# Optimization experiments

Measured on AMD Instinct MI355X. Metric: run time of the kernel, lower is better.

## Reference

```python
import jax, jax.numpy as jnp
import numpy as np

W_KERNEL = 5      # dilation kernel size (w)
K_BG = 0.1        # background weight (k)
RELAX = 5.0       # sigmoid temperature (relax)
INF = 1e4         # 'no zero in column' sentinel (>> image diagonal)
EPS = 1e-7        # DiceLoss eps


def setup_inputs() -> dict:
    key = jax.random.key(0)
    k1, k2 = jax.random.split(key)
    B, H, W = 32, 256, 256
    preds = jax.random.normal(k1, (B, H, W), dtype=jnp.float32)
    targets = (jax.random.uniform(k2, (B, H, W)) > 0.99).astype(jnp.float32)
    return {"preds": preds, "targets": targets}


def _dilate(t, w):
    # cv2.dilate with w x w ones kernel == sliding-window max, SAME padding
    pad = w // 2
    return jax.lax.reduce_window(t, -jnp.inf, jax.lax.max,
                                 (1, w, w), (1, 1, 1),
                                 [(0, 0), (pad, pad), (pad, pad)])


def _vertical_dist(zero_mask):
    # per-column distance (in rows) to nearest zero pixel; [B,H,W] -> [B,H,W]
    B, H, W = zero_mask.shape
    rows = jnp.moveaxis(zero_mask, 1, 0)  # [H,B,W]

    def step(carry, z):
        d = jnp.where(z, 0.0, jnp.minimum(carry + 1.0, INF))
        return d, d

    init = jnp.full((B, W), INF, dtype=jnp.float32)
    _, fwd = jax.lax.scan(step, init, rows)
    _, bwd = jax.lax.scan(step, init, rows[::-1])
    g = jnp.minimum(fwd, bwd[::-1])  # [H,B,W]
    return jnp.moveaxis(g, 0, 1)


def _edt(fat):
    # exact euclidean distance transform (distance to nearest zero pixel),
    # separable two-pass: vertical 1D distance, then horizontal min-plus.
    B, H, W = fat.shape
    g = _vertical_dist(fat == 0)  # [B,H,W]
    col = jnp.arange(W, dtype=jnp.float32)
    off2 = (col[:, None] - col[None, :]) ** 2  # [W_j, W_k]

    def per_img(gi):  # gi: [H,W]
        # d2[i,j] = min_k g[i,k]^2 + (j-k)^2   -> [H,W,W] intermediate
        d2 = jnp.min(gi[:, None, :] ** 2 + off2[None, :, :], axis=-1)
        return jnp.sqrt(d2)

    return jax.lax.map(per_img, g)  # sequential over batch caps memory


def _distance_maps(targets):
    fat = _dilate(targets, W_KERNEL)          # [B,H,W]
    d = _edt(fat)                              # [B,H,W]
    soft = jax.nn.sigmoid(d / RELAX)
    soft = soft - jnp.min(soft, axis=(1, 2), keepdims=True)
    mx = jnp.max(soft, axis=(1, 2), keepdims=True)
    soft = soft / jnp.where(mx > 0, mx, 1.0)
    dm_soft = soft + (1.0 - fat) * K_BG
    has_fg = jnp.max(targets, axis=(1, 2), keepdims=True) > 0
    return jnp.where(has_fg, dm_soft, 1.0 - targets)


def reference(preds, targets):
    p = jax.nn.sigmoid(preds)
    dm = jax.lax.stop_gradient(_distance_maps(targets))  # computed in numpy in torch => constant
    pw = p * dm
    bs = pw.shape[0]
    y_pred = pw.reshape(bs, 1, -1)
    y_true = targets.reshape(bs, 1, -1)
    # smp DiceLoss('binary', from_logits=False): dims=(0,2), smooth=0, eps=1e-7
    inter = jnp.sum(y_pred * y_true, axis=(0, 2))
    card = jnp.sum(y_pred + y_true, axis=(0, 2))
    dice = (2.0 * inter) / jnp.maximum(card, EPS)
    loss = 1.0 - dice
    mask = (jnp.sum(y_true, axis=(0, 2)) > 0).astype(loss.dtype)
    return jnp.mean(loss * mask)
```

## Files before the change

kernel.cpp:

```cpp
#include <hip/hip_runtime.h>
#include <math.h>

#define BB 32
#define HH 256
#define WW 256
#define HW (HH*WW)
#define K_BG 0.1f
#define RELAX 5.0f
#define EPS_D 1e-7

typedef unsigned long long u64;
typedef unsigned short u16;

__device__ __forceinline__ float sigf(float x) { return 1.0f / (1.0f + expf(-x)); }

__device__ __forceinline__ u64 shflx64(u64 x, int s) {
    return (u64)__shfl_xor((unsigned long long)x, s, 64);
}

__global__ void k_maskdil(const float* __restrict__ tg, u64* __restrict__ dmaskT,
                          u64* __restrict__ nzmask) {
    __shared__ u64 nz[20][4];
    __shared__ u64 hd[20][4];
    int blk = blockIdx.x;
    int b = blk >> 4, band = blk & 15;
    int r0 = band * 16;
    int t = threadIdx.x, w = t >> 6;
    const float* img = tg + b * HW;
    for (int rr = 0; rr < 20; ++rr) {
        int rg = r0 + rr - 2;
        float v = (rg >= 0 && rg < HH) ? img[rg * WW + t] : 0.0f;
        u64 bal = __ballot(v != 0.0f);
        if ((t & 63) == 0) nz[rr][w] = bal;
    }
    __syncthreads();
    if (t < 80) {
        int rr = t >> 2, k = t & 3;
        u64 m = nz[rr][k];
        u64 ml = (k > 0) ? nz[rr][k - 1] : 0ULL;
        u64 mr = (k < 3) ? nz[rr][k + 1] : 0ULL;
        hd[rr][k] = m | (m << 1) | (m << 2) | (m >> 1) | (m >> 2)
                  | (ml >> 62) | (ml >> 63) | (mr << 62) | (mr << 63);
    }
    if (t < 64) {
        int rr = t >> 2, k = t & 3;
        nzmask[b * 1024 + (r0 + rr) * 4 + k] = nz[rr + 2][k];
    }
    __syncthreads();
    if (t < 64) {
        int rr = t >> 2, k = t & 3;
        u64 o = hd[rr][k] | hd[rr + 1][k] | hd[rr + 2][k] | hd[rr + 3][k] | hd[rr + 4][k];
        dmaskT[b * 1024 + k * 256 + (r0 + rr)] = o;
    }
}

__global__ __launch_bounds__(256) void k_mega(const float* __restrict__ preds,
                                              const u64* __restrict__ dmaskT,
                                              const u64* __restrict__ nzmask,
                                              float4* __restrict__ part1,
                                              float4* __restrict__ part2) {
    __shared__ u64 colT[4 * 256];
    __shared__ u16 gS[4][WW];
    __shared__ float red[8][4];
    int blk = blockIdx.x;
    int b = blk >> 6, q = blk & 63;
    int i0 = q * 4;
    int tid = threadIdx.x;
    int lane = tid & 63, wv = tid >> 6;
    int j = tid;

    float p[4];
    u64 nzw[4];
    #pragma unroll
    for (int rr = 0; rr < 4; ++rr) {
        p[rr] = preds[(b * HH + i0 + rr) * WW + j];
        nzw[rr] = nzmask[b * 1024 + (i0 + rr) * 4 + (j >> 6)];
    }

    const u64* base = dmaskT + b * 1024;
    const u64 L32 = 0x00000000FFFFFFFFULL, L16 = 0x0000FFFF0000FFFFULL,
              L8  = 0x00FF00FF00FF00FFULL, L4  = 0x0F0F0F0F0F0F0F0FULL,
              L2  = 0x3333333333333333ULL, L1  = 0x5555555555555555ULL;
    #pragma unroll
    for (int w = 0; w < 4; ++w) {
        u64 x = base[w * 256 + wv * 64 + lane];
        u64 pp;
        pp = shflx64(x, 32); x = (lane & 32) ? ((x & ~L32) | ((pp & ~L32) >> 32)) : ((x & L32) | ((pp & L32) << 32));
        pp = shflx64(x, 16); x = (lane & 16) ? ((x & ~L16) | ((pp & ~L16) >> 16)) : ((x & L16) | ((pp & L16) << 16));
        pp = shflx64(x,  8); x = (lane &  8) ? ((x & ~L8 ) | ((pp & ~L8 ) >>  8)) : ((x & L8 ) | ((pp & L8 ) <<  8));
        pp = shflx64(x,  4); x = (lane &  4) ? ((x & ~L4 ) | ((pp & ~L4 ) >>  4)) : ((x & L4 ) | ((pp & L4 ) <<  4));
        pp = shflx64(x,  2); x = (lane &  2) ? ((x & ~L2 ) | ((pp & ~L2 ) >>  2)) : ((x & L2 ) | ((pp & L2 ) <<  2));
        pp = shflx64(x,  1); x = (lane &  1) ? ((x & ~L1 ) | ((pp & ~L1 ) >>  1)) : ((x & L1 ) | ((pp & L1 ) <<  1));
        colT[wv * 256 + w * 64 + lane] = x;
    }
    __syncthreads();

    u64 yw[4];
    #pragma unroll
    for (int g = 0; g < 4; ++g) yw[g] = ~colT[g * 256 + j];

    int g0v[4], fgv[4];
    #pragma unroll
    for (int rr = 0; rr < 4; ++rr) {
        int i = i0 + rr;
        int iw = i >> 6, ib = i & 63;
        u64 lowm  = (2ULL << ib) - 1ULL;
        u64 highm = ~((1ULL << ib) - 1ULL);
        int pu = -1, pd = -1;
        #pragma unroll
        for (int w = 0; w < 4; ++w) {
            u64 m = (w < iw) ? ~0ULL : ((w == iw) ? lowm : 0ULL);
            u64 z = yw[w] & m;
            int cand = (w << 6) + 63 - __clzll(z);
            pu = z ? cand : pu;
        }
        #pragma unroll
        for (int w = 3; w >= 0; --w) {
            u64 m = (w > iw) ? ~0ULL : ((w == iw) ? highm : 0ULL);
            u64 z = yw[w] & m;
            int cand = (w << 6) + (__ffsll((unsigned long long)z) - 1);
            pd = z ? cand : pd;
        }
        int up = (pu >= 0) ? (i - pu) : 10000;
        int dn = (pd >= 0) ? (pd - i) : 10000;
        int g0 = min(min(up, dn), 10000);
        g0v[rr] = g0;
        fgv[rr] = (int)((~yw[iw] >> ib) & 1ULL);
        gS[rr][j] = (u16)g0;
    }
    __syncthreads();

    float vals[8];
    #pragma unroll
    for (int qq = 0; qq < 6; ++qq) vals[qq] = 0.0f;
    vals[6] = 1e30f; vals[7] = 0.0f;
    #pragma unroll
    for (int rr = 0; rr < 4; ++rr) {
        float gv = (float)g0v[rr];
        float best = gv * gv;
        for (int r = 1; r < WW; ++r) {
            float rf = (float)(r * r);
            if (rf >= best) break;
            int jl = j - r, jr = j + r;
            if (jl >= 0) { float v = (float)gS[rr][jl]; best = fminf(best, v * v + rf); }
            if (jr < WW) { float v = (float)gS[rr][jr]; best = fminf(best, v * v + rf); }
        }
        float dv = sqrtf(best);
        float sp = sigf(p[rr]);
        float sd = sigf(dv / RELAX);
        float tv = (float)((nzw[rr] >> (j & 63)) & 1ULL);
        vals[0] += sp * sd * tv;
        vals[1] += sp * tv;
        vals[2] += sp * sd;
        vals[3] += sp;
        vals[4] += fgv[rr] ? 0.0f : sp;
        vals[5] += tv;
        vals[6] = fminf(vals[6], dv);
        vals[7] = fmaxf(vals[7], dv);
    }
    for (int off = 32; off > 0; off >>= 1) {
        #pragma unroll
        for (int qq = 0; qq < 6; ++qq) vals[qq] += __shfl_down(vals[qq], off, 64);
        vals[6] = fminf(vals[6], __shfl_down(vals[6], off, 64));
        vals[7] = fmaxf(vals[7], __shfl_down(vals[7], off, 64));
    }
    if (lane == 0) {
        #pragma unroll
        for (int qq = 0; qq < 8; ++qq) red[qq][wv] = vals[qq];
    }
    __syncthreads();
    if (tid == 0) {
        float s[8];
        #pragma unroll
        for (int qq = 0; qq < 6; ++qq) s[qq] = red[qq][0] + red[qq][1] + red[qq][2] + red[qq][3];
        s[6] = fminf(fminf(red[6][0], red[6][1]), fminf(red[6][2], red[6][3]));
        s[7] = fmaxf(fmaxf(red[7][0], red[7][1]), fmaxf(red[7][2], red[7][3]));
        part1[blk] = make_float4(s[0], s[1], s[2], s[3]);
        part2[blk] = make_float4(s[4], s[5], s[6], s[7]);
    }
}

__global__ void k_img(const float4* __restrict__ part1, const float4* __restrict__ part2,
                      float4* __restrict__ imgout) {
    int b = blockIdx.x, t = threadIdx.x;
    float4 p1 = part1[b * 64 + t];
    float4 p2 = part2[b * 64 + t];
    float vals[8] = {p1.x, p1.y, p1.z, p1.w, p2.x, p2.y, p2.z, p2.w};
    for (int off = 32; off > 0; off >>= 1) {
        #pragma unroll
        for (int qq = 0; qq < 6; ++qq) vals[qq] += __shfl_down(vals[qq], off, 64);
        vals[6] = fminf(vals[6], __shfl_down(vals[6], off, 64));
        vals[7] = fmaxf(vals[7], __shfl_down(vals[7], off, 64));
    }
    if (t == 0) {
        float A = vals[0], Bs = vals[1], Ap = vals[2], Bp = vals[3];
        float Cp = vals[4], T = vals[5], dmn = vals[6], dmx = vals[7];
        float inter, card, any;
        if (dmx > 0.0f) {
            float smin = sigf(dmn / RELAX);
            float smax = sigf(dmx / RELAX);
            float m = smax - smin;
            float denom = (m > 0.0f) ? m : 1.0f;
            inter = (A - smin * Bs) / denom;
            card  = (Ap - smin * Bp) / denom + K_BG * Cp + T;
            any = 1.0f;
        } else {
            inter = 0.0f;
            card = Bp - Bs + T;
            any = 0.0f;
        }
        imgout[b] = make_float4(inter, card, any, 0.0f);
    }
}

__global__ void k_fin(const float4* __restrict__ imgout, float* __restrict__ out) {
    if (threadIdx.x == 0) {
        double I = 0.0, C = 0.0;
        int any = 0;
        for (int b = 0; b < BB; ++b) {
            float4 v = imgout[b];
            I += (double)v.x; C += (double)v.y;
            any |= (v.z > 0.0f);
        }
        double dice = 2.0 * I / fmax(C, (double)EPS_D);
        out[0] = any ? (float)(1.0 - dice) : 0.0f;
    }
}

extern "C" void kernel_launch(void* const* d_in, const int* in_sizes, int n_in,
                              void* d_out, int out_size, void* d_ws, size_t ws_size,
                              hipStream_t stream) {
    const float* preds = (const float*)d_in[0];
    const float* tg    = (const float*)d_in[1];
    float* out = (float*)d_out;

    u64* dmaskT   = (u64*)d_ws;
    u64* nzmask   = dmaskT + BB * 1024;
    float4* part1 = (float4*)(nzmask + BB * 1024);
    float4* part2 = part1 + BB * 64;
    float4* imgout = part2 + BB * 64;

    hipLaunchKernelGGL(k_maskdil, dim3(BB * 16), dim3(WW), 0, stream, tg, dmaskT, nzmask);
    hipLaunchKernelGGL(k_mega, dim3(BB * 64), dim3(WW), 0, stream, preds, dmaskT, nzmask,
                       part1, part2);
    hipLaunchKernelGGL(k_img, dim3(BB), dim3(64), 0, stream, part1, part2, imgout);
    hipLaunchKernelGGL(k_fin, dim3(1), dim3(64), 0, stream, imgout, out);
}
```

Baseline: 95.81 us.

## Hoist column-mask transpose into its own kernel, double rows per block, merge tail kernels

Result: no change. 96.25 us (+0.5%).

```diff
diff --git a/kernel.cpp b/kernel.cpp
--- a/kernel.cpp
+++ b/kernel.cpp
@@ -8,6 +8,7 @@
 #define K_BG 0.1f
 #define RELAX 5.0f
 #define EPS_D 1e-7
+#define RPB 8
 
 typedef unsigned long long u64;
 typedef unsigned short u16;
@@ -54,29 +55,9 @@
     }
 }
 
-__global__ __launch_bounds__(256) void k_mega(const float* __restrict__ preds,
-                                              const u64* __restrict__ dmaskT,
-                                              const u64* __restrict__ nzmask,
-                                              float4* __restrict__ part1,
-                                              float4* __restrict__ part2) {
-    __shared__ u64 colT[4 * 256];
-    __shared__ u16 gS[4][WW];
-    __shared__ float red[8][4];
-    int blk = blockIdx.x;
-    int b = blk >> 6, q = blk & 63;
-    int i0 = q * 4;
-    int tid = threadIdx.x;
-    int lane = tid & 63, wv = tid >> 6;
-    int j = tid;
-
-    float p[4];
-    u64 nzw[4];
-    #pragma unroll
-    for (int rr = 0; rr < 4; ++rr) {
-        p[rr] = preds[(b * HH + i0 + rr) * WW + j];
-        nzw[rr] = nzmask[b * 1024 + (i0 + rr) * 4 + (j >> 6)];
-    }
-
+__global__ void k_transp(const u64* __restrict__ dmaskT, u64* __restrict__ cmask) {
+    int b = blockIdx.x;
+    int tid = threadIdx.x, lane = tid & 63, wv = tid >> 6;
     const u64* base = dmaskT + b * 1024;
     const u64 L32 = 0x00000000FFFFFFFFULL, L16 = 0x0000FFFF0000FFFFULL,
               L8  = 0x00FF00FF00FF00FFULL, L4  = 0x0F0F0F0F0F0F0F0FULL,
@@ -91,17 +72,38 @@
         pp = shflx64(x,  4); x = (lane &  4) ? ((x & ~L4 ) | ((pp & ~L4 ) >>  4)) : ((x & L4 ) | ((pp & L4 ) <<  4));
         pp = shflx64(x,  2); x = (lane &  2) ? ((x & ~L2 ) | ((pp & ~L2 ) >>  2)) : ((x & L2 ) | ((pp & L2 ) <<  2));
         pp = shflx64(x,  1); x = (lane &  1) ? ((x & ~L1 ) | ((pp & ~L1 ) >>  1)) : ((x & L1 ) | ((pp & L1 ) <<  1));
-        colT[wv * 256 + w * 64 + lane] = x;
-    }
-    __syncthreads();
+        cmask[b * 1024 + (w * 64 + lane) * 4 + wv] = x;
+    }
+}
+
+__global__ __launch_bounds__(256) void k_mega(const float* __restrict__ preds,
+                                              const u64* __restrict__ cmask,
+                                              const u64* __restrict__ nzmask,
+                                              float4* __restrict__ part1,
+                                              float4* __restrict__ part2) {
+    __shared__ u16 gS[RPB][WW];
+    __shared__ float red[8][4];
+    int blk = blockIdx.x;
+    int b = blk >> 5, q = blk & 31;
+    int i0 = q * RPB;
+    int tid = threadIdx.x;
+    int lane = tid & 63, wv = tid >> 6;
+    int j = tid;
+
+    float p[RPB];
+    #pragma unroll
+    for (int rr = 0; rr < RPB; ++rr)
+        p[rr] = preds[(b * HH + i0 + rr) * WW + j];
 
     u64 yw[4];
-    #pragma unroll
-    for (int g = 0; g < 4; ++g) yw[g] = ~colT[g * 256 + j];
-
-    int g0v[4], fgv[4];
-    #pragma unroll
-    for (int rr = 0; rr < 4; ++rr) {
+    {
+        const u64* cm = cmask + b * 1024 + j * 4;
+        #pragma unroll
+        for (int g = 0; g < 4; ++g) yw[g] = ~cm[g];
+    }
+
+    #pragma unroll
+    for (int rr = 0; rr < RPB; ++rr) {
         int i = i0 + rr;
         int iw = i >> 6, ib = i & 63;
         u64 lowm  = (2ULL << ib) - 1ULL;
@@ -123,10 +125,7 @@
         }
         int up = (pu >= 0) ? (i - pu) : 10000;
         int dn = (pd >= 0) ? (pd - i) : 10000;
-        int g0 = min(min(up, dn), 10000);
-        g0v[rr] = g0;
-        fgv[rr] = (int)((~yw[iw] >> ib) & 1ULL);
-        gS[rr][j] = (u16)g0;
+        gS[rr][j] = (u16)min(min(up, dn), 10000);
     }
     __syncthreads();
 
@@ -135,8 +134,9 @@
     for (int qq = 0; qq < 6; ++qq) vals[qq] = 0.0f;
     vals[6] = 1e30f; vals[7] = 0.0f;
     #pragma unroll
-    for (int rr = 0; rr < 4; ++rr) {
-        float gv = (float)g0v[rr];
+    for (int rr = 0; rr < RPB; ++rr) {
+        int i = i0 + rr;
+        float gv = (float)gS[rr][j];
         float best = gv * gv;
         for (int r = 1; r < WW; ++r) {
             float rf = (float)(r * r);
@@ -148,12 +148,13 @@
         float dv = sqrtf(best);
         float sp = sigf(p[rr]);
         float sd = sigf(dv / RELAX);
-        float tv = (float)((nzw[rr] >> (j & 63)) & 1ULL);
+        float tv = (float)((nzmask[b * 1024 + i * 4 + wv] >> (j & 63)) & 1ULL);
+        int fg = (int)((~yw[i >> 6] >> (i & 63)) & 1ULL);
         vals[0] += sp * sd * tv;
         vals[1] += sp * tv;
         vals[2] += sp * sd;
         vals[3] += sp;
-        vals[4] += fgv[rr] ? 0.0f : sp;
+        vals[4] += fg ? 0.0f : sp;
         vals[5] += tv;
         vals[6] = fminf(vals[6], dv);
         vals[7] = fmaxf(vals[7], dv);
@@ -180,47 +181,50 @@
     }
 }
 
-__global__ void k_img(const float4* __restrict__ part1, const float4* __restrict__ part2,
-                      float4* __restrict__ imgout) {
-    int b = blockIdx.x, t = threadIdx.x;
-    float4 p1 = part1[b * 64 + t];
-    float4 p2 = part2[b * 64 + t];
-    float vals[8] = {p1.x, p1.y, p1.z, p1.w, p2.x, p2.y, p2.z, p2.w};
-    for (int off = 32; off > 0; off >>= 1) {
-        #pragma unroll
-        for (int qq = 0; qq < 6; ++qq) vals[qq] += __shfl_down(vals[qq], off, 64);
-        vals[6] = fminf(vals[6], __shfl_down(vals[6], off, 64));
-        vals[7] = fmaxf(vals[7], __shfl_down(vals[7], off, 64));
-    }
+__global__ void k_tail(const float4* __restrict__ part1, const float4* __restrict__ part2,
+                       float* __restrict__ out) {
+    __shared__ float sI[32], sC[32], sA[32];
+    int t = threadIdx.x;
+    #pragma unroll
+    for (int pass = 0; pass < 4; ++pass) {
+        int img = pass * 8 + (t >> 5);
+        int k = t & 31;
+        float4 p1 = part1[img * 32 + k];
+        float4 p2 = part2[img * 32 + k];
+        float vals[8] = {p1.x, p1.y, p1.z, p1.w, p2.x, p2.y, p2.z, p2.w};
+        for (int off = 16; off > 0; off >>= 1) {
+            #pragma unroll
+            for (int qq = 0; qq < 6; ++qq) vals[qq] += __shfl_down(vals[qq], off, 32);
+            vals[6] = fminf(vals[6], __shfl_down(vals[6], off, 32));
+            vals[7] = fmaxf(vals[7], __shfl_down(vals[7], off, 32));
+        }
+        if (k == 0) {
+            float A = vals[0], Bs = vals[1], Ap = vals[2], Bp = vals[3];
+            float Cp = vals[4], T = vals[5], dmn = vals[6], dmx = vals[7];
+            float inter, card, any;
+            if (dmx > 0.0f) {
+                float smin = sigf(dmn / RELAX);
+                float smax = sigf(dmx / RELAX);
+                float m = smax - smin;
+                float denom = (m > 0.0f) ? m : 1.0f;
+                inter = (A - smin * Bs) / denom;
+                card  = (Ap - smin * Bp) / denom + K_BG * Cp + T;
+                any = 1.0f;
+            } else {
+                inter = 0.0f;
+                card = Bp - Bs + T;
+                any = 0.0f;
+            }
+            sI[img] = inter; sC[img] = card; sA[img] = any;
+        }
+    }
+    __syncthreads();
     if (t == 0) {
-        float A = vals[0], Bs = vals[1], Ap = vals[2], Bp = vals[3];
-        float Cp = vals[4], T = vals[5], dmn = vals[6], dmx = vals[7];
-        float inter, card, any;
-        if (dmx > 0.0f) {
-            float smin = sigf(dmn / RELAX);
-            float smax = sigf(dmx / RELAX);
-            float m = smax - smin;
-            float denom = (m > 0.0f) ? m : 1.0f;
-            inter = (A - smin * Bs) / denom;
-            card  = (Ap - smin * Bp) / denom + K_BG * Cp + T;
-            any = 1.0f;
-        } else {
-            inter = 0.0f;
-            card = Bp - Bs + T;
-            any = 0.0f;
-        }
-        imgout[b] = make_float4(inter, card, any, 0.0f);
-    }
-}
-
-__global__ void k_fin(const float4* __restrict__ imgout, float* __restrict__ out) {
-    if (threadIdx.x == 0) {
         double I = 0.0, C = 0.0;
         int any = 0;
         for (int b = 0; b < BB; ++b) {
-            float4 v = imgout[b];
-            I += (double)v.x; C += (double)v.y;
-            any |= (v.z > 0.0f);
+            I += (double)sI[b]; C += (double)sC[b];
+            any |= (sA[b] > 0.0f);
         }
         double dice = 2.0 * I / fmax(C, (double)EPS_D);
         out[0] = any ? (float)(1.0 - dice) : 0.0f;
@@ -236,13 +240,13 @@
 
     u64* dmaskT   = (u64*)d_ws;
     u64* nzmask   = dmaskT + BB * 1024;
-    float4* part1 = (float4*)(nzmask + BB * 1024);
-    float4* part2 = part1 + BB * 64;
-    float4* imgout = part2 + BB * 64;
+    u64* cmask    = nzmask + BB * 1024;
+    float4* part1 = (float4*)(cmask + BB * 1024);
+    float4* part2 = part1 + BB * 32;
 
     hipLaunchKernelGGL(k_maskdil, dim3(BB * 16), dim3(WW), 0, stream, tg, dmaskT, nzmask);
-    hipLaunchKernelGGL(k_mega, dim3(BB * 64), dim3(WW), 0, stream, preds, dmaskT, nzmask,
+    hipLaunchKernelGGL(k_transp, dim3(BB), dim3(WW), 0, stream, dmaskT, cmask);
+    hipLaunchKernelGGL(k_mega, dim3(BB * 32), dim3(WW), 0, stream, preds, cmask, nzmask,
                        part1, part2);
-    hipLaunchKernelGGL(k_img, dim3(BB), dim3(64), 0, stream, part1, part2, imgout);
-    hipLaunchKernelGGL(k_fin, dim3(1), dim3(64), 0, stream, imgout, out);
-}
+    hipLaunchKernelGGL(k_tail, dim3(1), dim3(256), 0, stream, part1, part2, out);
+}
```
